# Performance work log

Hardware: AMD Instinct MI355X
Metric: run time of the kernel (lower is better)

Reference implementation:

```python
import jax, jax.numpy as jnp
import numpy as np

SENS = 200
DM = 128
NMAPS = 2
NLAYERS = 2
TH = 0.01
EPS = 1e-5
BATCH = 8
SEQ = 96
HEADS = 8


def setup_inputs() -> dict:
    key = jax.random.key(0)
    ks = jax.random.split(key, 8)
    x = jax.random.normal(ks[0], (BATCH, SENS, SEQ, DM), jnp.float32)
    attn_s = jax.random.uniform(ks[1], (1, BATCH, HEADS, SENS, SENS), jnp.float32)
    supports = jax.random.uniform(ks[2], (SENS, SENS), jnp.float32)
    W_conv = jax.random.normal(ks[3], (NMAPS, NLAYERS, DM, DM), jnp.float32) * 0.05
    b_conv = jnp.zeros((NMAPS, NLAYERS, DM), jnp.float32)
    bn_gamma = jnp.ones((NMAPS, DM), jnp.float32)
    bn_beta = jnp.zeros((NMAPS, DM), jnp.float32)
    W_out = jax.random.normal(ks[4], (NMAPS * DM, DM), jnp.float32) * 0.05
    b_out = jnp.zeros((DM,), jnp.float32)
    return dict(x=x, attn_s=attn_s, supports=supports, W_conv=W_conv,
                b_conv=b_conv, bn_gamma=bn_gamma, bn_beta=bn_beta,
                W_out=W_out, b_out=b_out)


def _process_map(A):
    # make_symmetric: lower triangle + mirrored strict lower triangle
    A = jnp.tril(A) + jnp.tril(A, -1).T
    # clamp: threshold on absolute value; note original returns |A| thresholded
    Aa = jnp.abs(A)
    A = jnp.where(Aa > TH, Aa, jnp.zeros_like(Aa))
    # SparseTensor.from_dense(A).t()
    return A.T


def _gcn_norm(adj_t):
    # GCNConv default: add self-loops (weight 1), symmetric D^-1/2 A D^-1/2
    A = adj_t + jnp.eye(adj_t.shape[0], dtype=adj_t.dtype)
    deg = A.sum(axis=1)
    d = jnp.where(deg > 0, jax.lax.rsqrt(deg), jnp.zeros_like(deg))
    return d[:, None] * A * d[None, :]


def reference(x, attn_s, supports, W_conv, b_conv, bn_gamma, bn_beta, W_out, b_out):
    B, N, S, D = x.shape
    # reshape_mat: [B,N,S,D] -> [B*S, N, D]
    xr = x.transpose(0, 2, 1, 3).reshape(B * S, N, D)

    # supports: [data map, adaptive map from attention (mean over batch, heads)]
    maps = [_process_map(supports), _process_map(attn_s[0].mean(axis=(0, 1)))]

    gcn_outputs = []
    for i in range(NMAPS):
        An = _gcn_norm(maps[i])  # [N,N]
        h = jnp.zeros_like(xr[..., :1]) * 0.0  # placeholder replaced below
        h = None
        for l in range(NLAYERS):
            xw = jnp.einsum('bnf,fg->bng', xr, W_conv[i, l])
            hl = jnp.einsum('mn,bng->bmg', An, xw) + b_conv[i, l]
            h = hl if h is None else h + hl
        # BatchNorm1d over feature channel (training-mode batch stats, biased var)
        mu = h.mean(axis=(0, 1))
        var = h.var(axis=(0, 1))
        hn = (h - mu) * jax.lax.rsqrt(var + EPS) * bn_gamma[i] + bn_beta[i]
        gcn_outputs.append(jax.nn.relu(hn))

    cat = jnp.concatenate(gcn_outputs, axis=-1)  # [B*S, N, NMAPS*DM]
    y = jax.nn.relu(jnp.einsum('bnc,cd->bnd', cat, W_out) + b_out)
    # inverse_reshape_mat: [B*S, N, D] -> [B, N, S, D]
    return y.reshape(B, S, N, D).transpose(0, 2, 1, 3)
```

## Files before the change

### kernel.cpp

```cpp
#include <hip/hip_runtime.h>

#define SENS 200
#define DM 128
#define SEQ 96
#define NB 8
#define BS 768
#define NTOT 153600
#define TH 0.01f
#define BN_EPS 1e-5f
#define MPAD 224
#define KP 208
#define XWS 212
#define ASROW 68

typedef __attribute__((ext_vector_type(8)))  __bf16 bf16x8;
typedef __attribute__((ext_vector_type(4)))  __bf16 bf16x4;
typedef __attribute__((ext_vector_type(16))) float  f32x16;

__device__ __forceinline__ f32x16 mfma32(bf16x8 a, bf16x8 b, f32x16 c) {
    return __builtin_amdgcn_mfma_f32_32x32x16_bf16(a, b, c, 0, 0, 0);
}
__device__ __forceinline__ bf16x8 join8(bf16x4 a, bf16x4 b) {
    bf16x8 r;
    #pragma unroll
    for (int j = 0; j < 4; ++j) { r[j] = a[j]; r[j + 4] = b[j]; }
    return r;
}

__global__ void attn_mean_kernel(const float* __restrict__ attn, float* __restrict__ mapA) {
    int idx = blockIdx.x * 256 + threadIdx.x;
    if (idx >= SENS * SENS) return;
    float s = 0.f;
    #pragma unroll 8
    for (int q = 0; q < 64; ++q) s += attn[(size_t)q * SENS * SENS + idx];
    mapA[idx] = s * (1.0f / 64.0f);
}

__global__ void build_map_kernel(const float* __restrict__ supports, const float* __restrict__ mapA,
                                 float* __restrict__ M, float* __restrict__ deg) {
    __shared__ float red[256];
    int m = blockIdx.x, map = blockIdx.y, j = threadIdx.x;
    const float* src = (map == 0) ? supports : mapA;
    float v = 0.f;
    if (j < SENS) {
        float sym = (m >= j) ? src[m * SENS + j] : src[j * SENS + m];
        float a = fabsf(sym);
        v = (a > TH) ? a : 0.f;
        M[(size_t)map * SENS * SENS + m * SENS + j] = v;
    }
    red[j] = v;
    __syncthreads();
    for (int off = 128; off > 0; off >>= 1) {
        if (j < off) red[j] += red[j + off];
        __syncthreads();
    }
    if (j == 0) deg[map * SENS + m] = red[0] + 1.0f;
}

__global__ __launch_bounds__(256) void prep2_kernel(
    const float* __restrict__ M, const float* __restrict__ deg,
    const float* __restrict__ W_conv, const float* __restrict__ b_conv,
    const float* __restrict__ W_out,
    __bf16* __restrict__ Anb, __bf16* __restrict__ Wt, __bf16* __restrict__ Wot,
    float* __restrict__ bsum, float* __restrict__ bnacc)
{
    const int bid = blockIdx.x, t = threadIdx.x;
    if (bid < 2 * MPAD) {
        const int map = bid / MPAD, m = bid % MPAD;
        const int j = t;
        if (j < KP) {
            float val = 0.f;
            if (m < SENS && j < SENS) {
                float a = M[((size_t)map * SENS + m) * SENS + j] + ((m == j) ? 1.f : 0.f);
                val = rsqrtf(deg[map * SENS + m]) * a * rsqrtf(deg[map * SENS + j]);
            }
            Anb[(((size_t)map * 13 + (j >> 4)) * MPAD + m) * 16 + (j & 15)] = (__bf16)val;
        }
    } else {
        const int idx = (bid - 2 * MPAD) * 256 + t;
        if (idx < 32768) {
            const int map = idx >> 14, g = (idx >> 7) & 127, f = idx & 127;
            const float* wp = W_conv + (size_t)map * 2 * DM * DM + f * DM + g;
            Wt[(((size_t)map * 8 + (f >> 4)) * DM + g) * 16 + (f & 15)] = (__bf16)(wp[0] + wp[DM * DM]);
        } else if (idx < 65536) {
            const int k = idx - 32768, d = k >> 8, c = k & 255;
            Wot[(((size_t)(c >> 4)) * DM + d) * 16 + (c & 15)] = (__bf16)W_out[c * DM + d];
        } else if (idx < 65792) {
            const int k = idx - 65536, map = k >> 7, g = k & 127;
            bsum[k] = b_conv[(map * 2) * DM + g] + b_conv[(map * 2 + 1) * DM + g];
        } else if (idx < 66304) {
            bnacc[idx - 65792] = 0.f;
        }
    }
}

__global__ __launch_bounds__(448, 4) void conv_kernel(
    const float* __restrict__ x, const __bf16* __restrict__ Anb,
    const __bf16* __restrict__ Wt, const float* __restrict__ bsum,
    __bf16* __restrict__ h, float* __restrict__ bnacc)
{
    __shared__ __bf16 xw[128 * XWS];
    const int bs = blockIdx.x;
    const int b = bs / SEQ, s = bs % SEQ;
    const int t = threadIdx.x, w = t >> 6, lane = t & 63;
    const int l31 = lane & 31, hi = lane >> 5;

    const int n = w * 32 + l31;
    const bool valid = (n < SENS);
    const float* xrow = x + (((size_t)b * SENS + (valid ? n : 0)) * SEQ + s) * DM + hi * 8;

    float bsn[2][4], bsq[2][4];

    #pragma unroll 1
    for (int map = 0; map < 2; ++map) {
        if (map) __syncthreads();
        {
            f32x16 acc[4];
            #pragma unroll
            for (int gt = 0; gt < 4; ++gt)
                #pragma unroll
                for (int r = 0; r < 16; ++r) acc[gt][r] = 0.f;
            const __bf16* wb = Wt + (((size_t)map * 8) * DM + l31) * 16 + hi * 8;
            #pragma unroll
            for (int kc = 0; kc < 8; ++kc) {
                float4 v0 = *(const float4*)(xrow + kc * 16);
                float4 v1 = *(const float4*)(xrow + kc * 16 + 4);
                bf16x8 bfrag;
                bfrag[0] = (__bf16)v0.x; bfrag[1] = (__bf16)v0.y;
                bfrag[2] = (__bf16)v0.z; bfrag[3] = (__bf16)v0.w;
                bfrag[4] = (__bf16)v1.x; bfrag[5] = (__bf16)v1.y;
                bfrag[6] = (__bf16)v1.z; bfrag[7] = (__bf16)v1.w;
                if (!valid) {
                    #pragma unroll
                    for (int j = 0; j < 8; ++j) bfrag[j] = (__bf16)0.f;
                }
                const __bf16* wp = wb + (size_t)kc * DM * 16;
                #pragma unroll
                for (int gt = 0; gt < 4; ++gt)
                    acc[gt] = mfma32(*(const bf16x8*)(wp + gt * 32 * 16), bfrag, acc[gt]);
            }
            if (n < KP) {
                #pragma unroll
                for (int gt = 0; gt < 4; ++gt)
                    #pragma unroll
                    for (int r = 0; r < 16; ++r) {
                        const int g = gt * 32 + (r & 3) + 8 * (r >> 2) + 4 * hi;
                        xw[g * XWS + n] = (__bf16)acc[gt][r];
                    }
            }
        }
        __syncthreads();

        f32x16 acc2[4];
        #pragma unroll
        for (int gt = 0; gt < 4; ++gt)
            #pragma unroll
            for (int r = 0; r < 16; ++r) acc2[gt][r] = 0.f;
        {
            const __bf16* ab = Anb + (((size_t)map * 13) * MPAD + w * 32 + l31) * 16 + hi * 8;
            #pragma unroll 2
            for (int kc = 0; kc < 13; ++kc) {
                bf16x8 afrag = *(const bf16x8*)(ab + (size_t)kc * MPAD * 16);
                #pragma unroll
                for (int gt = 0; gt < 4; ++gt) {
                    bf16x8 bfrag = *(const bf16x8*)(xw + (gt * 32 + l31) * XWS + kc * 16 + hi * 8);
                    acc2[gt] = mfma32(afrag, bfrag, acc2[gt]);
                }
            }
        }
        #pragma unroll
        for (int gt = 0; gt < 4; ++gt) {
            const float bias = bsum[map * DM + gt * 32 + l31];
            bf16x8 h0, h1;
            float s2 = 0.f, q = 0.f;
            #pragma unroll
            for (int r = 0; r < 16; ++r) {
                const float v = acc2[gt][r] + bias;
                if (r < 8) h0[r] = (__bf16)v; else h1[r - 8] = (__bf16)v;
                const int m = w * 32 + (r & 3) + 8 * (r >> 2) + 4 * hi;
                if (m < SENS) { s2 += v; q += v * v; }
            }
            __bf16* hp = h + ((((size_t)(bs * 2 + map) * 7 + w) * 4 + gt) * 64 + lane) * 16;
            *(bf16x8*)hp = h0;
            *(bf16x8*)(hp + 8) = h1;
            s2 += __shfl_xor(s2, 32);
            q += __shfl_xor(q, 32);
            bsn[map][gt] = s2; bsq[map][gt] = q;
        }
    }
    __syncthreads();
    float* red = (float*)xw;
    if (hi == 0) {
        #pragma unroll
        for (int map = 0; map < 2; ++map)
            #pragma unroll
            for (int gt = 0; gt < 4; ++gt) {
                red[(((map * 2 + 0) * 128) + gt * 32 + l31) * 7 + w] = bsn[map][gt];
                red[(((map * 2 + 1) * 128) + gt * 32 + l31) * 7 + w] = bsq[map][gt];
            }
    }
    __syncthreads();
    for (int i = t; i < 512; i += 448) {
        const int map = i >> 8, sq = (i >> 7) & 1, g = i & 127;
        float s2 = 0.f;
        #pragma unroll
        for (int k = 0; k < 7; ++k) s2 += red[i * 7 + k];
        atomicAdd(&bnacc[sq * 256 + map * DM + g], s2);
    }
}

__device__ __forceinline__ void out_stage(int cn, int t, int bs,
                                          const __bf16* __restrict__ h,
                                          const float* sc_s, const float* sh_s,
                                          __bf16* dst)
{
    const int mapn = cn >> 1;
    const __bf16* hb = h + ((size_t)(bs * 2 + mapn) * 28 + (cn & 1) * 2) * 1024;
    bf16x8 vv[4];
    #pragma unroll
    for (int it = 0; it < 4; ++it) {
        const int idx = it * 512 + t;
        if (idx < 1792)
            vv[it] = *(const bf16x8*)(hb + ((size_t)(idx >> 8) * 4 + ((idx >> 7) & 1)) * 1024
                                          + ((idx >> 1) & 63) * 16 + (idx & 1) * 8);
    }
    #pragma unroll
    for (int it = 0; it < 4; ++it) {
        const int idx = it * 512 + t;
        if (idx < 1792) {
            const int half = idx & 1, lane_s = (idx >> 1) & 63;
            const int ctl = (idx >> 7) & 1, strip = idx >> 8;
            const int cl = ctl * 32 + (lane_s & 31);
            const int cg = mapn * DM + (cn & 1) * 64 + cl;
            const float scv = sc_s[cg], shv = sh_s[cg];
            const int mbase = strip * 32 + 4 * (lane_s >> 5) + 16 * half;
            #pragma unroll
            for (int q2 = 0; q2 < 8; ++q2) {
                const int row = mbase + (q2 & 3) + 8 * (q2 >> 2);
                const float fv = (float)vv[it][q2] * scv + shv;
                dst[row * ASROW + cl] = (__bf16)fmaxf(fv, 0.f);
            }
        }
    }
}

__global__ __launch_bounds__(512) void out_kernel(
    const __bf16* __restrict__ h, const __bf16* __restrict__ Wot,
    const float* __restrict__ bnacc,
    const float* __restrict__ gamma, const float* __restrict__ beta,
    const float* __restrict__ b_out, float* __restrict__ out)
{
    __shared__ __bf16 As[2][MPAD * ASROW];
    __shared__ float sc_s[256], sh_s[256];
    const int bs = blockIdx.x;
    const int b = bs / SEQ, s = bs % SEQ;
    const int t = threadIdx.x, w = t >> 6, lane = t & 63;
    const int l31 = lane & 31, hi = lane >> 5;
    const int dct = w & 3, sbase = w >> 2;
    if (t < 256) {
        const float mu = bnacc[t] * (1.f / (float)NTOT);
        const float var = bnacc[256 + t] * (1.f / (float)NTOT) - mu * mu;
        const float sc = gamma[t] * rsqrtf(var + BN_EPS);
        sc_s[t] = sc;
        sh_s[t] = beta[t] - mu * sc;
    }
    f32x16 acc[4];
    {
        const float bo = b_out[dct * 32 + l31];
        #pragma unroll
        for (int i = 0; i < 4; ++i)
            #pragma unroll
            for (int r = 0; r < 16; ++r) acc[i][r] = bo;
    }
    __syncthreads();
    out_stage(0, t, bs, h, sc_s, sh_s, &As[0][0]);
    __syncthreads();
    for (int c = 0; c < 4; ++c) {
        #pragma unroll
        for (int kc = 0; kc < 4; ++kc) {
            bf16x8 bfrag = *(const bf16x8*)(Wot + ((size_t)(c * 4 + kc) * DM + dct * 32 + l31) * 16 + hi * 8);
            #pragma unroll
            for (int i = 0; i < 4; ++i) {
                const int strip = sbase + 2 * i;
                if (strip >= 7) break;
                const __bf16* ap = &As[c & 1][(strip * 32 + l31) * ASROW + kc * 16 + hi * 8];
                acc[i] = mfma32(join8(*(const bf16x4*)ap, *(const bf16x4*)(ap + 4)), bfrag, acc[i]);
            }
        }
        if (c < 3) out_stage(c + 1, t, bs, h, sc_s, sh_s, &As[(c + 1) & 1][0]);
        __syncthreads();
    }
    #pragma unroll
    for (int i = 0; i < 4; ++i) {
        const int strip = sbase + 2 * i;
        if (strip >= 7) break;
        #pragma unroll
        for (int r = 0; r < 16; ++r) {
            const int m = strip * 32 + (r & 3) + 8 * (r >> 2) + 4 * hi;
            if (m < SENS)
                out[(((size_t)b * SENS + m) * SEQ + s) * DM + dct * 32 + l31] = fmaxf(acc[i][r], 0.f);
        }
    }
}

extern "C" void kernel_launch(void* const* d_in, const int* in_sizes, int n_in,
                              void* d_out, int out_size, void* d_ws, size_t ws_size,
                              hipStream_t stream) {
    const float* x        = (const float*)d_in[0];
    const float* attn     = (const float*)d_in[1];
    const float* supports = (const float*)d_in[2];
    const float* W_conv   = (const float*)d_in[3];
    const float* b_conv   = (const float*)d_in[4];
    const float* gamma    = (const float*)d_in[5];
    const float* beta     = (const float*)d_in[6];
    const float* W_out    = (const float*)d_in[7];
    const float* b_out    = (const float*)d_in[8];
    float* out = (float*)d_out;
    char* base = (char*)d_ws;

    float*  mapA  = (float*)(base + 0);
    float*  Mbuf  = (float*)(base + 160000);
    float*  deg   = (float*)(base + 480000);
    float*  bnacc = (float*)(base + 481664);
    float*  bsum  = (float*)(base + 483712);
    __bf16* Wt    = (__bf16*)(base + 484736);
    __bf16* Wot   = (__bf16*)(base + 550272);
    __bf16* Anb   = (__bf16*)(base + 615808);
    __bf16* h     = (__bf16*)(base + 1048576);

    attn_mean_kernel<<<157, 256, 0, stream>>>(attn, mapA);
    build_map_kernel<<<dim3(SENS, 2), 256, 0, stream>>>(supports, mapA, Mbuf, deg);
    prep2_kernel<<<2 * MPAD + 260, 256, 0, stream>>>(Mbuf, deg, W_conv, b_conv, W_out,
                                                     Anb, Wt, Wot, bsum, bnacc);
    conv_kernel<<<BS, 448, 0, stream>>>(x, Anb, Wt, bsum, h, bnacc);
    out_kernel<<<BS, 512, 0, stream>>>(h, Wot, bnacc, gamma, beta, b_out, out);
}
```

Measured before the change: 261.3 us.

## Restructure conv kernel to keep XW in registers via permlane swaps

The conv kernel is reorganized so that each of 4 waves owns a 32-column output-feature slice. x is staged once into LDS as bf16, and the XW product is converted in registers into B-fragments for the adjacency GEMM using v_permlane32_swap, with no LDS round-trip. The reduction for the BatchNorm statistics moves from an LDS-based cross-wave sum to direct per-lane atomics. The change removes an LDS store/sync phase, but it uses more registers (13 fragments plus 7 accumulators) with fewer threads per block and adds more global atomics.

```diff
diff --git a/kernel.cpp b/kernel.cpp
--- a/kernel.cpp
+++ b/kernel.cpp
@@ -3,14 +3,13 @@
 #define SENS 200
 #define DM 128
 #define SEQ 96
-#define NB 8
 #define BS 768
 #define NTOT 153600
 #define TH 0.01f
 #define BN_EPS 1e-5f
 #define MPAD 224
 #define KP 208
-#define XWS 212
+#define XSS 132
 #define ASROW 68
 
 typedef __attribute__((ext_vector_type(8)))  __bf16 bf16x8;
@@ -25,6 +24,19 @@
     #pragma unroll
     for (int j = 0; j < 4; ++j) { r[j] = a[j]; r[j + 4] = b[j]; }
     return r;
+}
+__device__ __forceinline__ unsigned pk2(float a, float b) {
+    union { unsigned u; __bf16 hh[2]; } t;
+    t.hh[0] = (__bf16)a; t.hh[1] = (__bf16)b;
+    return t.u;
+}
+__device__ __forceinline__ void permswap(unsigned &a, unsigned &b) {
+    asm("v_permlane32_swap_b32 %0, %1" : "+v"(a), "+v"(b));
+}
+__device__ __forceinline__ bf16x8 frag4(unsigned a, unsigned b, unsigned c, unsigned d) {
+    union { unsigned u[4]; bf16x8 v; } t;
+    t.u[0] = a; t.u[1] = b; t.u[2] = c; t.u[3] = d;
+    return t.v;
 }
 
 __global__ void attn_mean_kernel(const float* __restrict__ attn, float* __restrict__ mapA) {
@@ -94,118 +106,104 @@
     }
 }
 
-__global__ __launch_bounds__(448, 4) void conv_kernel(
+__global__ __launch_bounds__(256, 2) void conv_kernel(
     const float* __restrict__ x, const __bf16* __restrict__ Anb,
     const __bf16* __restrict__ Wt, const float* __restrict__ bsum,
     __bf16* __restrict__ h, float* __restrict__ bnacc)
 {
-    __shared__ __bf16 xw[128 * XWS];
+    __shared__ __bf16 xs[MPAD * XSS];
     const int bs = blockIdx.x;
     const int b = bs / SEQ, s = bs % SEQ;
-    const int t = threadIdx.x, w = t >> 6, lane = t & 63;
+    const int t = threadIdx.x;
+    const int wt = t >> 6, lane = t & 63;
     const int l31 = lane & 31, hi = lane >> 5;
 
-    const int n = w * 32 + l31;
-    const bool valid = (n < SENS);
-    const float* xrow = x + (((size_t)b * SENS + (valid ? n : 0)) * SEQ + s) * DM + hi * 8;
-
-    float bsn[2][4], bsq[2][4];
+    {
+        const float* xb = x + ((size_t)b * SENS * SEQ + s) * DM;
+        for (int i = t; i < SENS * 32; i += 256) {
+            const int n = i >> 5, c = i & 31;
+            const float4 v = *(const float4*)(xb + (size_t)n * SEQ * DM + c * 4);
+            union { uint2 u; __bf16 hh[4]; } p;
+            p.hh[0] = (__bf16)v.x; p.hh[1] = (__bf16)v.y;
+            p.hh[2] = (__bf16)v.z; p.hh[3] = (__bf16)v.w;
+            *(uint2*)(&xs[n * XSS + c * 4]) = p.u;
+        }
+        unsigned* zp = (unsigned*)(&xs[SENS * XSS]);
+        for (int i = t; i < (MPAD - SENS) * (XSS / 2); i += 256) zp[i] = 0u;
+    }
+    __syncthreads();
 
     #pragma unroll 1
     for (int map = 0; map < 2; ++map) {
-        if (map) __syncthreads();
+        bf16x8 wf[8];
         {
-            f32x16 acc[4];
-            #pragma unroll
-            for (int gt = 0; gt < 4; ++gt)
+            const __bf16* wb = Wt + (((size_t)map * 8) * DM + wt * 32 + l31) * 16 + hi * 8;
+            #pragma unroll
+            for (int k = 0; k < 8; ++k) wf[k] = *(const bf16x8*)(wb + (size_t)k * DM * 16);
+        }
+        bf16x8 xwf[13];
+        #pragma unroll
+        for (int nt = 0; nt < 7; ++nt) {
+            f32x16 acc;
+            #pragma unroll
+            for (int r = 0; r < 16; ++r) acc[r] = 0.f;
+            const __bf16* xp = &xs[(nt * 32 + l31) * XSS + hi * 8];
+            #pragma unroll
+            for (int k = 0; k < 8; ++k)
+                acc = mfma32(*(const bf16x8*)(xp + k * 16), wf[k], acc);
+            {
+                unsigned w0 = pk2(acc[0], acc[1]),  w1 = pk2(acc[2], acc[3]);
+                unsigned w2 = pk2(acc[4], acc[5]),  w3 = pk2(acc[6], acc[7]);
+                permswap(w0, w2); permswap(w1, w3);
+                xwf[2 * nt] = frag4(w0, w1, w2, w3);
+            }
+            if (nt < 6) {
+                unsigned w0 = pk2(acc[8], acc[9]),   w1 = pk2(acc[10], acc[11]);
+                unsigned w2 = pk2(acc[12], acc[13]), w3 = pk2(acc[14], acc[15]);
+                permswap(w0, w2); permswap(w1, w3);
+                xwf[2 * nt + 1] = frag4(w0, w1, w2, w3);
+            }
+        }
+
+        f32x16 acc2[7];
+        #pragma unroll
+        for (int mt = 0; mt < 7; ++mt)
+            #pragma unroll
+            for (int r = 0; r < 16; ++r) acc2[mt][r] = 0.f;
+        {
+            const __bf16* ab = Anb + (((size_t)map * 13) * MPAD + l31) * 16 + hi * 8;
+            #pragma unroll
+            for (int kc = 0; kc < 13; ++kc) {
                 #pragma unroll
-                for (int r = 0; r < 16; ++r) acc[gt][r] = 0.f;
-            const __bf16* wb = Wt + (((size_t)map * 8) * DM + l31) * 16 + hi * 8;
-            #pragma unroll
-            for (int kc = 0; kc < 8; ++kc) {
-                float4 v0 = *(const float4*)(xrow + kc * 16);
-                float4 v1 = *(const float4*)(xrow + kc * 16 + 4);
-                bf16x8 bfrag;
-                bfrag[0] = (__bf16)v0.x; bfrag[1] = (__bf16)v0.y;
-                bfrag[2] = (__bf16)v0.z; bfrag[3] = (__bf16)v0.w;
-                bfrag[4] = (__bf16)v1.x; bfrag[5] = (__bf16)v1.y;
-                bfrag[6] = (__bf16)v1.z; bfrag[7] = (__bf16)v1.w;
-                if (!valid) {
-                    #pragma unroll
-                    for (int j = 0; j < 8; ++j) bfrag[j] = (__bf16)0.f;
+                for (int mt = 0; mt < 7; ++mt) {
+                    const bf16x8 af = *(const bf16x8*)(ab + ((size_t)kc * MPAD + mt * 32) * 16);
+                    acc2[mt] = mfma32(af, xwf[kc], acc2[mt]);
                 }
-                const __bf16* wp = wb + (size_t)kc * DM * 16;
-                #pragma unroll
-                for (int gt = 0; gt < 4; ++gt)
-                    acc[gt] = mfma32(*(const bf16x8*)(wp + gt * 32 * 16), bfrag, acc[gt]);
-            }
-            if (n < KP) {
-                #pragma unroll
-                for (int gt = 0; gt < 4; ++gt)
-                    #pragma unroll
-                    for (int r = 0; r < 16; ++r) {
-                        const int g = gt * 32 + (r & 3) + 8 * (r >> 2) + 4 * hi;
-                        xw[g * XWS + n] = (__bf16)acc[gt][r];
-                    }
-            }
-        }
-        __syncthreads();
-
-        f32x16 acc2[4];
-        #pragma unroll
-        for (int gt = 0; gt < 4; ++gt)
-            #pragma unroll
-            for (int r = 0; r < 16; ++r) acc2[gt][r] = 0.f;
-        {
-            const __bf16* ab = Anb + (((size_t)map * 13) * MPAD + w * 32 + l31) * 16 + hi * 8;
-            #pragma unroll 2
-            for (int kc = 0; kc < 13; ++kc) {
-                bf16x8 afrag = *(const bf16x8*)(ab + (size_t)kc * MPAD * 16);
-                #pragma unroll
-                for (int gt = 0; gt < 4; ++gt) {
-                    bf16x8 bfrag = *(const bf16x8*)(xw + (gt * 32 + l31) * XWS + kc * 16 + hi * 8);
-                    acc2[gt] = mfma32(afrag, bfrag, acc2[gt]);
-                }
-            }
-        }
-        #pragma unroll
-        for (int gt = 0; gt < 4; ++gt) {
-            const float bias = bsum[map * DM + gt * 32 + l31];
+            }
+        }
+
+        const float bias = bsum[map * DM + wt * 32 + l31];
+        float sv = 0.f, qv = 0.f;
+        #pragma unroll
+        for (int mt = 0; mt < 7; ++mt) {
             bf16x8 h0, h1;
-            float s2 = 0.f, q = 0.f;
             #pragma unroll
             for (int r = 0; r < 16; ++r) {
-                const float v = acc2[gt][r] + bias;
+                const float v = acc2[mt][r] + bias;
                 if (r < 8) h0[r] = (__bf16)v; else h1[r - 8] = (__bf16)v;
-                const int m = w * 32 + (r & 3) + 8 * (r >> 2) + 4 * hi;
-                if (m < SENS) { s2 += v; q += v * v; }
-            }
-            __bf16* hp = h + ((((size_t)(bs * 2 + map) * 7 + w) * 4 + gt) * 64 + lane) * 16;
+                const int m = mt * 32 + (r & 3) + 8 * (r >> 2) + 4 * hi;
+                if (m < SENS) { sv += v; qv += v * v; }
+            }
+            __bf16* hp = h + ((((size_t)(bs * 2 + map) * 7 + mt) * 4 + wt) * 64 + lane) * 16;
             *(bf16x8*)hp = h0;
             *(bf16x8*)(hp + 8) = h1;
-            s2 += __shfl_xor(s2, 32);
-            q += __shfl_xor(q, 32);
-            bsn[map][gt] = s2; bsq[map][gt] = q;
-        }
-    }
-    __syncthreads();
-    float* red = (float*)xw;
-    if (hi == 0) {
-        #pragma unroll
-        for (int map = 0; map < 2; ++map)
-            #pragma unroll
-            for (int gt = 0; gt < 4; ++gt) {
-                red[(((map * 2 + 0) * 128) + gt * 32 + l31) * 7 + w] = bsn[map][gt];
-                red[(((map * 2 + 1) * 128) + gt * 32 + l31) * 7 + w] = bsq[map][gt];
-            }
-    }
-    __syncthreads();
-    for (int i = t; i < 512; i += 448) {
-        const int map = i >> 8, sq = (i >> 7) & 1, g = i & 127;
-        float s2 = 0.f;
-        #pragma unroll
-        for (int k = 0; k < 7; ++k) s2 += red[i * 7 + k];
-        atomicAdd(&bnacc[sq * 256 + map * DM + g], s2);
+        }
+        sv += __shfl_xor(sv, 32);
+        qv += __shfl_xor(qv, 32);
+        if (hi == 0) {
+            atomicAdd(&bnacc[map * DM + wt * 32 + l31], sv);
+            atomicAdd(&bnacc[256 + map * DM + wt * 32 + l31], qv);
+        }
     }
 }
 
@@ -332,6 +330,6 @@
     build_map_kernel<<<dim3(SENS, 2), 256, 0, stream>>>(supports, mapA, Mbuf, deg);
     prep2_kernel<<<2 * MPAD + 260, 256, 0, stream>>>(Mbuf, deg, W_conv, b_conv, W_out,
                                                      Anb, Wt, Wot, bsum, bnacc);
-    conv_kernel<<<BS, 448, 0, stream>>>(x, Anb, Wt, bsum, h, bnacc);
+    conv_kernel<<<BS, 256, 0, stream>>>(x, Anb, Wt, bsum, h, bnacc);
     out_kernel<<<BS, 512, 0, stream>>>(h, Wot, bnacc, gamma, beta, b_out, out);
 }
```

After: 276.8 us. +5.9%, slower.

## Split conv kernel output channels into halves to cut LDS and registers

Applied to the files above, without the earlier changes.

The conv kernel now processes each map in two 64-channel halves, four passes instead of two. This halves the xw shared buffer and the accumulator register count, and the launch-bounds occupancy hint rises from 4 to 7 blocks. Batch-norm partial sums are reduced per pass through a small shared buffer and pushed with atomics. The cost is that the x rows are reloaded and converted to bf16 twice as often, the A-matrix fragments are re-read per half, and there are more block-wide barriers.

```diff
diff --git a/kernel.cpp b/kernel.cpp
--- a/kernel.cpp
+++ b/kernel.cpp
@@ -94,12 +94,13 @@
     }
 }
 
-__global__ __launch_bounds__(448, 4) void conv_kernel(
+__global__ __launch_bounds__(448, 7) void conv_kernel(
     const float* __restrict__ x, const __bf16* __restrict__ Anb,
     const __bf16* __restrict__ Wt, const float* __restrict__ bsum,
     __bf16* __restrict__ h, float* __restrict__ bnacc)
 {
-    __shared__ __bf16 xw[128 * XWS];
+    __shared__ __bf16 xw[64 * XWS];
+    __shared__ float bnred[2 * 7 * 64];
     const int bs = blockIdx.x;
     const int b = bs / SEQ, s = bs % SEQ;
     const int t = threadIdx.x, w = t >> 6, lane = t & 63;
@@ -109,18 +110,25 @@
     const bool valid = (n < SENS);
     const float* xrow = x + (((size_t)b * SENS + (valid ? n : 0)) * SEQ + s) * DM + hi * 8;
 
-    float bsn[2][4], bsq[2][4];
-
     #pragma unroll 1
-    for (int map = 0; map < 2; ++map) {
-        if (map) __syncthreads();
+    for (int mh = 0; mh < 4; ++mh) {
+        const int map = mh >> 1, gh = mh & 1;
+        if (mh) __syncthreads();
+        if (mh && t < 128) {
+            const int pm = (mh - 1) >> 1, pg = (mh - 1) & 1;
+            const int sq = t >> 6, gl = t & 63;
+            float ssum = 0.f;
+            #pragma unroll
+            for (int k = 0; k < 7; ++k) ssum += bnred[(sq * 7 + k) * 64 + gl];
+            atomicAdd(&bnacc[sq * 256 + pm * DM + pg * 64 + gl], ssum);
+        }
         {
-            f32x16 acc[4];
-            #pragma unroll
-            for (int gt = 0; gt < 4; ++gt)
+            f32x16 acc[2];
+            #pragma unroll
+            for (int gt2 = 0; gt2 < 2; ++gt2)
                 #pragma unroll
-                for (int r = 0; r < 16; ++r) acc[gt][r] = 0.f;
-            const __bf16* wb = Wt + (((size_t)map * 8) * DM + l31) * 16 + hi * 8;
+                for (int r = 0; r < 16; ++r) acc[gt2][r] = 0.f;
+            const __bf16* wb = Wt + (((size_t)map * 8) * DM + gh * 64 + l31) * 16 + hi * 8;
             #pragma unroll
             for (int kc = 0; kc < 8; ++kc) {
                 float4 v0 = *(const float4*)(xrow + kc * 16);
@@ -135,47 +143,47 @@
                     for (int j = 0; j < 8; ++j) bfrag[j] = (__bf16)0.f;
                 }
                 const __bf16* wp = wb + (size_t)kc * DM * 16;
-                #pragma unroll
-                for (int gt = 0; gt < 4; ++gt)
-                    acc[gt] = mfma32(*(const bf16x8*)(wp + gt * 32 * 16), bfrag, acc[gt]);
+                acc[0] = mfma32(*(const bf16x8*)wp, bfrag, acc[0]);
+                acc[1] = mfma32(*(const bf16x8*)(wp + 32 * 16), bfrag, acc[1]);
             }
             if (n < KP) {
                 #pragma unroll
-                for (int gt = 0; gt < 4; ++gt)
+                for (int gt2 = 0; gt2 < 2; ++gt2)
                     #pragma unroll
                     for (int r = 0; r < 16; ++r) {
-                        const int g = gt * 32 + (r & 3) + 8 * (r >> 2) + 4 * hi;
-                        xw[g * XWS + n] = (__bf16)acc[gt][r];
+                        const int gl = gt2 * 32 + (r & 3) + 8 * (r >> 2) + 4 * hi;
+                        xw[gl * XWS + n] = (__bf16)acc[gt2][r];
                     }
             }
         }
         __syncthreads();
 
-        f32x16 acc2[4];
-        #pragma unroll
-        for (int gt = 0; gt < 4; ++gt)
-            #pragma unroll
-            for (int r = 0; r < 16; ++r) acc2[gt][r] = 0.f;
+        f32x16 acc2[2];
+        #pragma unroll
+        for (int gt2 = 0; gt2 < 2; ++gt2)
+            #pragma unroll
+            for (int r = 0; r < 16; ++r) acc2[gt2][r] = 0.f;
         {
             const __bf16* ab = Anb + (((size_t)map * 13) * MPAD + w * 32 + l31) * 16 + hi * 8;
             #pragma unroll 2
             for (int kc = 0; kc < 13; ++kc) {
                 bf16x8 afrag = *(const bf16x8*)(ab + (size_t)kc * MPAD * 16);
                 #pragma unroll
-                for (int gt = 0; gt < 4; ++gt) {
-                    bf16x8 bfrag = *(const bf16x8*)(xw + (gt * 32 + l31) * XWS + kc * 16 + hi * 8);
-                    acc2[gt] = mfma32(afrag, bfrag, acc2[gt]);
+                for (int gt2 = 0; gt2 < 2; ++gt2) {
+                    bf16x8 bfrag = *(const bf16x8*)(xw + (gt2 * 32 + l31) * XWS + kc * 16 + hi * 8);
+                    acc2[gt2] = mfma32(afrag, bfrag, acc2[gt2]);
                 }
             }
         }
         #pragma unroll
-        for (int gt = 0; gt < 4; ++gt) {
+        for (int gt2 = 0; gt2 < 2; ++gt2) {
+            const int gt = gh * 2 + gt2;
             const float bias = bsum[map * DM + gt * 32 + l31];
             bf16x8 h0, h1;
             float s2 = 0.f, q = 0.f;
             #pragma unroll
             for (int r = 0; r < 16; ++r) {
-                const float v = acc2[gt][r] + bias;
+                const float v = acc2[gt2][r] + bias;
                 if (r < 8) h0[r] = (__bf16)v; else h1[r - 8] = (__bf16)v;
                 const int m = w * 32 + (r & 3) + 8 * (r >> 2) + 4 * hi;
                 if (m < SENS) { s2 += v; q += v * v; }
@@ -184,28 +192,20 @@
             *(bf16x8*)hp = h0;
             *(bf16x8*)(hp + 8) = h1;
             s2 += __shfl_xor(s2, 32);
-            q += __shfl_xor(q, 32);
-            bsn[map][gt] = s2; bsq[map][gt] = q;
+            q  += __shfl_xor(q, 32);
+            if (hi == 0) {
+                bnred[(0 * 7 + w) * 64 + gt2 * 32 + l31] = s2;
+                bnred[(1 * 7 + w) * 64 + gt2 * 32 + l31] = q;
+            }
         }
     }
     __syncthreads();
-    float* red = (float*)xw;
-    if (hi == 0) {
-        #pragma unroll
-        for (int map = 0; map < 2; ++map)
-            #pragma unroll
-            for (int gt = 0; gt < 4; ++gt) {
-                red[(((map * 2 + 0) * 128) + gt * 32 + l31) * 7 + w] = bsn[map][gt];
-                red[(((map * 2 + 1) * 128) + gt * 32 + l31) * 7 + w] = bsq[map][gt];
-            }
-    }
-    __syncthreads();
-    for (int i = t; i < 512; i += 448) {
-        const int map = i >> 8, sq = (i >> 7) & 1, g = i & 127;
-        float s2 = 0.f;
-        #pragma unroll
-        for (int k = 0; k < 7; ++k) s2 += red[i * 7 + k];
-        atomicAdd(&bnacc[sq * 256 + map * DM + g], s2);
+    if (t < 128) {
+        const int sq = t >> 6, gl = t & 63;
+        float ssum = 0.f;
+        #pragma unroll
+        for (int k = 0; k < 7; ++k) ssum += bnred[(sq * 7 + k) * 64 + gl];
+        atomicAdd(&bnacc[sq * 256 + DM + 64 + gl], ssum);
     }
 }
 
```

Result: slower. 273.2 us (+4.6%).
